# Kernel optimization log

Measured on AMD Instinct MI355X. Metric: run time of the kernel, lower is better.

## Reference

```python
import jax, jax.numpy as jnp
import numpy as np


def setup_inputs() -> dict:
    key = jax.random.key(0)
    k1, k2 = jax.random.split(key)
    inputs = jax.random.normal(k1, (32768, 512), dtype=jnp.float32)
    codebook = jax.random.normal(k2, (8192, 512), dtype=jnp.float32)
    return {"inputs": inputs, "codebook": codebook}


def reference(inputs, codebook):
    # inputs: [N, D] (flattened), codebook: [K, D]
    D = codebook.shape[1]
    x = inputs.reshape(-1, D)                          # [N, D]
    cb_sqr = jnp.sum(codebook ** 2, axis=1)            # [K]
    x_sqr = jnp.sum(x ** 2, axis=1, keepdims=True)     # [N, 1]
    distances = (cb_sqr[None, :] + x_sqr) - 2.0 * jnp.einsum('nd,kd->nk', x, codebook)
    soft_distances = jax.nn.softmax(-distances, axis=1)  # [N, K]
    return soft_distances
```

## Files before the change

kernel.cpp:

```cpp
#include <hip/hip_runtime.h>


typedef __attribute__((ext_vector_type(8))) __bf16 bf16x8;
typedef __attribute__((ext_vector_type(4))) float f32x4;

typedef __attribute__((address_space(1))) const void global_cvoid;
typedef __attribute__((address_space(3))) void lds_void;

__device__ inline unsigned short f32_to_bf16_rne(float f) {
    unsigned int u = __float_as_uint(f);
    unsigned int r = u + 0x7FFFu + ((u >> 16) & 1u);
    return (unsigned short)(r >> 16);
}
__device__ inline float bf16u_to_f32(unsigned short h) {
    return __uint_as_float(((unsigned int)h) << 16);
}

__global__ void split_kernel(const float* __restrict__ in,
                             unsigned short* __restrict__ hi,
                             unsigned short* __restrict__ lo, int n4) {
    int i = blockIdx.x * blockDim.x + threadIdx.x;
    int stride = gridDim.x * blockDim.x;
    for (; i < n4; i += stride) {
        float4 v = reinterpret_cast<const float4*>(in)[i];
        float vv[4] = {v.x, v.y, v.z, v.w};
        ushort4 hv, lv;
        unsigned short h[4], l[4];
#pragma unroll
        for (int j = 0; j < 4; ++j) {
            h[j] = f32_to_bf16_rne(vv[j]);
            float r = vv[j] - bf16u_to_f32(h[j]);
            l[j] = f32_to_bf16_rne(r);
        }
        hv.x = h[0]; hv.y = h[1]; hv.z = h[2]; hv.w = h[3];
        lv.x = l[0]; lv.y = l[1]; lv.z = l[2]; lv.w = l[3];
        reinterpret_cast<ushort4*>(hi)[i] = hv;
        reinterpret_cast<ushort4*>(lo)[i] = lv;
    }
}

__global__ void rowsq_kernel(const float* __restrict__ cb, float* __restrict__ out) {
    int row = blockIdx.x * 4 + (threadIdx.x >> 6);
    int lane = threadIdx.x & 63;
    const float4* p = reinterpret_cast<const float4*>(cb + (size_t)row * 512);
    float4 a = p[lane];
    float4 b = p[lane + 64];
    float s = a.x * a.x + a.y * a.y + a.z * a.z + a.w * a.w +
              b.x * b.x + b.y * b.y + b.z * b.z + b.w * b.w;
#pragma unroll
    for (int o = 32; o >= 1; o >>= 1) s += __shfl_xor(s, o);
    if (lane == 0) out[row] = s;
}


#define RD_A(mq_, kk_, b_)                                                        \
    { _Pragma("unroll") for (int m = 0; m < 4; ++m)                               \
        afr[m] = *(const bf16x8*)&lds[b_][0][kk_][(a_slot + ((mq_)*4 + m) * 64) * 8]; }

#define RD_B(kk_, b_)                                                             \
    { _Pragma("unroll") for (int n = 0; n < 4; ++n)                               \
        bfr[n] = *(const bf16x8*)&lds[b_][1][kk_][(b_slot + n * 64) * 8]; }

#define ST(mat_, kk_, b_, tt_)                                                    \
    { int prod_ = (tt_) >> 3, ch_ = (tt_) & 7;                                    \
      const unsigned short* bse_;                                                 \
      if ((mat_) == 0) bse_ = (prod_ < 2 ? Ah : Al) + arow0;                      \
      else             bse_ = (prod_ == 1 ? Bl : Bh) + brow0;                     \
      bse_ += ch_ * 64 + (kk_) * 32;                                              \
      _Pragma("unroll") for (int j = 0; j < 2; ++j)                               \
          __builtin_amdgcn_global_load_lds((global_cvoid*)(bse_ + goff[j]),       \
              (lds_void*)&lds[b_][mat_][kk_][sl8[j]], 16, 0, 0);                  \
    }

#define MM(mq_)                                                                   \
    { _Pragma("unroll") for (int m = 0; m < 4; ++m)                               \
      _Pragma("unroll") for (int n = 0; n < 4; ++n)                               \
          acc[(mq_) * 4 + m][n] = __builtin_amdgcn_mfma_f32_16x16x32_bf16(        \
              afr[m], bfr[n], acc[(mq_) * 4 + m][n], 0, 0, 0); }

#define MIDSYNC()                                                                 \
    { __builtin_amdgcn_s_barrier();                                               \
      asm volatile("s_waitcnt lgkmcnt(0)" ::: "memory"); }

template <int F16>
__global__ __launch_bounds__(512, 2) void gemm_kernel(
    const unsigned short* __restrict__ Ah, const unsigned short* __restrict__ Al,
    const unsigned short* __restrict__ Bh, const unsigned short* __restrict__ Bl,
    const float* __restrict__ cbq, float* __restrict__ outf,
    unsigned short* __restrict__ p16, float* __restrict__ max_part,
    float* __restrict__ sum_part) {
    __shared__ __align__(16) unsigned short lds[2][2][2][8192];

    const int t = threadIdx.x;
    const int lane = t & 63;
    const int w = t >> 6;
    const int wm = w >> 2, wn = w & 3;
    const int fr = lane & 15, fg = lane >> 4;

    int bid = blockIdx.x;
    int swz = (bid & 7) * 512 + (bid >> 3);
    const int bm = swz >> 5, bn = swz & 31;
    const int row0 = bm * 256, col0 = bn * 256;
    const size_t arow0 = (size_t)row0 * 512;
    const size_t brow0 = (size_t)col0 * 512;

    const int xsl = fg ^ ((fr >> 1) & 3);
    const int a_slot = (wm * 128 + fr) * 4 + xsl;
    const int b_slot = (wn * 64 + fr) * 4 + xsl;

    int goff[2], sl8[2];
#pragma unroll
    for (int j = 0; j < 2; ++j) {
        int s = j * 512 + t;
        int r_ = s >> 2, cp_ = s & 3;
        int cl_ = cp_ ^ ((r_ >> 1) & 3);
        goff[j] = r_ * 512 + cl_ * 8;
        sl8[j] = s * 8;
    }

    f32x4 acc[8][4] = {};
    bf16x8 afr[4], bfr[4];

    ST(0, 0, 0, 0);
    ST(1, 0, 0, 0);
    ST(0, 1, 0, 0);
    ST(1, 1, 0, 0);
    asm volatile("s_waitcnt vmcnt(4)\n\ts_barrier" ::: "memory");

    for (int tt = 0; tt < 24; ++tt) {
        const int cur = tt & 1, nb = cur ^ 1;
        const bool pf = (tt < 23);
        RD_B(0, cur);
        RD_A(0, 0, cur);
        if (pf) ST(0, 0, nb, tt + 1);
        MIDSYNC();
        __builtin_amdgcn_s_setprio(1); MM(0); __builtin_amdgcn_s_setprio(0);
        __builtin_amdgcn_s_barrier();
        RD_A(1, 0, cur);
        if (pf) ST(1, 0, nb, tt + 1);
        MIDSYNC();
        __builtin_amdgcn_s_setprio(1); MM(1); __builtin_amdgcn_s_setprio(0);
        if (pf) {
            asm volatile("s_waitcnt vmcnt(4)\n\ts_barrier" ::: "memory");
        } else {
            asm volatile("s_waitcnt vmcnt(0)\n\ts_barrier" ::: "memory");
        }
        RD_B(1, cur);
        RD_A(0, 1, cur);
        if (pf) ST(0, 1, nb, tt + 1);
        MIDSYNC();
        __builtin_amdgcn_s_setprio(1); MM(0); __builtin_amdgcn_s_setprio(0);
        __builtin_amdgcn_s_barrier();
        RD_A(1, 1, cur);
        if (pf) ST(1, 1, nb, tt + 1);
        MIDSYNC();
        __builtin_amdgcn_s_setprio(1); MM(1); __builtin_amdgcn_s_setprio(0);
        if (pf) {
            asm volatile("s_waitcnt vmcnt(4)\n\ts_barrier" ::: "memory");
        } else {
            __builtin_amdgcn_s_barrier();
        }
    }

    float* redm = (float*)&lds[0][0][0][0];
    float* reds = redm + 1024;

    float cq[4];
#pragma unroll
    for (int n = 0; n < 4; ++n) cq[n] = cbq[col0 + wn * 64 + n * 16 + fr];
#pragma unroll
    for (int m = 0; m < 8; ++m)
#pragma unroll
        for (int n = 0; n < 4; ++n)
#pragma unroll
            for (int r = 0; r < 4; ++r)
                acc[m][n][r] = 2.0f * acc[m][n][r] - cq[n];

    float rmx[8][4];
#pragma unroll
    for (int m = 0; m < 8; ++m)
#pragma unroll
        for (int r = 0; r < 4; ++r) {
            float v = fmaxf(fmaxf(acc[m][0][r], acc[m][1][r]),
                            fmaxf(acc[m][2][r], acc[m][3][r]));
#pragma unroll
            for (int o = 1; o < 16; o <<= 1) v = fmaxf(v, __shfl_xor(v, o));
            rmx[m][r] = v;
        }
    __syncthreads();
    if (fr == 0) {
#pragma unroll
        for (int m = 0; m < 8; ++m)
#pragma unroll
            for (int r = 0; r < 4; ++r)
                redm[wn * 256 + wm * 128 + m * 16 + fg * 4 + r] = rmx[m][r];
    }
    __syncthreads();
#pragma unroll
    for (int m = 0; m < 8; ++m)
#pragma unroll
        for (int r = 0; r < 4; ++r) {
            int row = wm * 128 + m * 16 + fg * 4 + r;
            rmx[m][r] = fmaxf(fmaxf(redm[row], redm[256 + row]),
                              fmaxf(redm[512 + row], redm[768 + row]));
        }
#pragma unroll
    for (int m = 0; m < 8; ++m)
#pragma unroll
        for (int r = 0; r < 4; ++r) {
            float s = 0.f;
#pragma unroll
            for (int n = 0; n < 4; ++n) s += __expf(acc[m][n][r] - rmx[m][r]);
#pragma unroll
            for (int o = 1; o < 16; o <<= 1) s += __shfl_xor(s, o);
            if (fr == 0) reds[wn * 256 + wm * 128 + m * 16 + fg * 4 + r] = s;
        }
    __syncthreads();
    if (wn == 0 && fr == 0) {
#pragma unroll
        for (int m = 0; m < 8; ++m)
#pragma unroll
            for (int r = 0; r < 4; ++r) {
                int row = wm * 128 + m * 16 + fg * 4 + r;
                size_t gr = (size_t)(row0 + row);
                max_part[gr * 32 + bn] = rmx[m][r];
                sum_part[gr * 32 + bn] =
                    reds[row] + reds[256 + row] + reds[512 + row] + reds[768 + row];
            }
    }
#pragma unroll
    for (int m = 0; m < 8; ++m)
#pragma unroll
        for (int n = 0; n < 4; ++n)
#pragma unroll
            for (int r = 0; r < 4; ++r) {
                size_t gr = (size_t)(row0 + wm * 128 + m * 16 + fg * 4 + r);
                size_t gi = gr * 8192 + col0 + wn * 64 + n * 16 + fr;
                if constexpr (F16) {
                    union { _Float16 h; unsigned short u; } cv;
                    cv.h = (_Float16)__expf(acc[m][n][r] - rmx[m][r]);
                    p16[gi] = cv.u;
                } else {
                    outf[gi] = acc[m][n][r];
                }
            }
}

__global__ void combine_kernel(const float* __restrict__ max_part,
                               const float* __restrict__ sum_part,
                               float* __restrict__ row_m, float* __restrict__ row_is,
                               float* __restrict__ scale, int do_scale) {
    int row = blockIdx.x * 8 + (threadIdx.x >> 5);
    int l = threadIdx.x & 31;
    size_t off = (size_t)row * 32 + l;
    float m = max_part[off];
    float s = sum_part[off];
    float gm = m;
#pragma unroll
    for (int o = 16; o >= 1; o >>= 1) gm = fmaxf(gm, __shfl_xor(gm, o, 32));
    float c = s * __expf(m - gm);
#pragma unroll
    for (int o = 16; o >= 1; o >>= 1) c += __shfl_xor(c, o, 32);
    float inv = 1.0f / c;
    if (do_scale) scale[off] = __expf(m - gm) * inv;
    if (l == 0) {
        row_m[row] = gm;
        row_is[row] = inv;
    }
}

__global__ void norm_kernel(float* __restrict__ out, const float* __restrict__ row_m,
                            const float* __restrict__ row_is) {
    size_t i = (size_t)blockIdx.x * blockDim.x + threadIdx.x;
    size_t stride = (size_t)gridDim.x * blockDim.x;
    const size_t n4 = 268435456ull / 4;
    float4* p = reinterpret_cast<float4*>(out);
    for (; i < n4; i += stride) {
        int row = (int)(i >> 11);
        float m = row_m[row];
        float is = row_is[row];
        float4 v = p[i];
        v.x = __expf(v.x - m) * is;
        v.y = __expf(v.y - m) * is;
        v.z = __expf(v.z - m) * is;
        v.w = __expf(v.w - m) * is;
        p[i] = v;
    }
}

__global__ void norm_f16_kernel(const unsigned short* __restrict__ p16,
                                const float* __restrict__ scale,
                                float* __restrict__ out) {
    size_t i = (size_t)blockIdx.x * blockDim.x + threadIdx.x;
    size_t stride = (size_t)gridDim.x * blockDim.x;
    const size_t ng = 268435456ull / 8;
    const uint4* src = reinterpret_cast<const uint4*>(p16);
    float4* dst = reinterpret_cast<float4*>(out);
    for (; i < ng; i += stride) {
        int row = (int)(i >> 10);
        int bn = (int)((i >> 5) & 31);
        float s = scale[(size_t)row * 32 + bn];
        union { uint4 u; _Float16 h[8]; } cv;
        cv.u = src[i];
        float4 o1, o2;
        o1.x = (float)cv.h[0] * s; o1.y = (float)cv.h[1] * s;
        o1.z = (float)cv.h[2] * s; o1.w = (float)cv.h[3] * s;
        o2.x = (float)cv.h[4] * s; o2.y = (float)cv.h[5] * s;
        o2.z = (float)cv.h[6] * s; o2.w = (float)cv.h[7] * s;
        dst[i * 2] = o1;
        dst[i * 2 + 1] = o2;
    }
}

extern "C" void kernel_launch(void* const* d_in, const int* in_sizes, int n_in,
                              void* d_out, int out_size, void* d_ws, size_t ws_size,
                              hipStream_t stream) {
    const float* x = (const float*)d_in[0];
    const float* cb = (const float*)d_in[1];
    float* out = (float*)d_out;
    char* ws = (char*)d_ws;

    unsigned short* Xh = (unsigned short*)(ws);
    unsigned short* Xl = (unsigned short*)(ws + 33554432ull);
    unsigned short* Ch = (unsigned short*)(ws + 67108864ull);
    unsigned short* Cl = (unsigned short*)(ws + 75497472ull);
    float* cbq       = (float*)(ws + 83886080ull);
    float* max_part  = (float*)(ws + 83918848ull);
    float* sum_part  = (float*)(ws + 88113152ull);
    float* row_m     = (float*)(ws + 92307456ull);
    float* row_is    = (float*)(ws + 92438528ull);
    float* scale     = (float*)(ws + 92569600ull);
    unsigned short* p16 = (unsigned short*)(ws + 96763904ull);

    const bool f16path = (ws_size >= 633634816ull);

    split_kernel<<<2048, 256, 0, stream>>>(x, Xh, Xl, 32768 * 512 / 4);
    split_kernel<<<1024, 256, 0, stream>>>(cb, Ch, Cl, 8192 * 512 / 4);
    rowsq_kernel<<<2048, 256, 0, stream>>>(cb, cbq);
    if (f16path) {
        gemm_kernel<1><<<4096, 512, 0, stream>>>(Xh, Xl, Ch, Cl, cbq, out, p16,
                                                 max_part, sum_part);
        combine_kernel<<<4096, 256, 0, stream>>>(max_part, sum_part, row_m, row_is,
                                                 scale, 1);
        norm_f16_kernel<<<4096, 256, 0, stream>>>(p16, scale, out);
    } else {
        gemm_kernel<0><<<4096, 512, 0, stream>>>(Xh, Xl, Ch, Cl, cbq, out, p16,
                                                 max_part, sum_part);
        combine_kernel<<<4096, 256, 0, stream>>>(max_part, sum_part, row_m, row_is,
                                                 scale, 0);
        norm_kernel<<<4096, 256, 0, stream>>>(out, row_m, row_is);
    }
}
```

Before: 1.380 ms.

## Deepen GEMM LDS pipeline to four stages with three tiles in flight

Replaces the double-buffered K-loop (two 32-wide sub-chunks per buffer) with a four-slot ring of 32-wide K chunks. Each step issues the A and B loads together three chunks ahead and waits with vmcnt(8), so more global-to-LDS loads are in flight while the MFMAs run. Total LDS size stays the same, but the loop now has 48 shorter iterations and a hand-tuned wait/barrier tail, which must stay correct for the last three chunks.

```diff
diff --git a/kernel.cpp b/kernel.cpp
--- a/kernel.cpp
+++ b/kernel.cpp
@@ -53,24 +53,24 @@
 }
 
 
-#define RD_A(mq_, kk_, b_)                                                        \
+#define RD_A(mq_, bq_)                                                            \
     { _Pragma("unroll") for (int m = 0; m < 4; ++m)                               \
-        afr[m] = *(const bf16x8*)&lds[b_][0][kk_][(a_slot + ((mq_)*4 + m) * 64) * 8]; }
-
-#define RD_B(kk_, b_)                                                             \
+        afr[m] = *(const bf16x8*)&lds[bq_][0][(a_slot + ((mq_)*4 + m) * 64) * 8]; }
+
+#define RD_B(bq_)                                                                 \
     { _Pragma("unroll") for (int n = 0; n < 4; ++n)                               \
-        bfr[n] = *(const bf16x8*)&lds[b_][1][kk_][(b_slot + n * 64) * 8]; }
-
-#define ST(mat_, kk_, b_, tt_)                                                    \
-    { int prod_ = (tt_) >> 3, ch_ = (tt_) & 7;                                    \
-      const unsigned short* bse_;                                                 \
-      if ((mat_) == 0) bse_ = (prod_ < 2 ? Ah : Al) + arow0;                      \
-      else             bse_ = (prod_ == 1 ? Bl : Bh) + brow0;                     \
-      bse_ += ch_ * 64 + (kk_) * 32;                                              \
-      _Pragma("unroll") for (int j = 0; j < 2; ++j)                               \
-          __builtin_amdgcn_global_load_lds((global_cvoid*)(bse_ + goff[j]),       \
-              (lds_void*)&lds[b_][mat_][kk_][sl8[j]], 16, 0, 0);                  \
-    }
+        bfr[n] = *(const bf16x8*)&lds[bq_][1][(b_slot + n * 64) * 8]; }
+
+#define ST(tt_)                                                                   \
+    { int prod_ = (tt_) >> 4, ko_ = ((tt_) & 15) * 32, bq_ = (tt_) & 3;           \
+      const unsigned short* Asrc_ = (prod_ < 2 ? Ah : Al) + arow0 + ko_;          \
+      const unsigned short* Bsrc_ = (prod_ == 1 ? Bl : Bh) + brow0 + ko_;         \
+      _Pragma("unroll") for (int j = 0; j < 2; ++j) {                             \
+          __builtin_amdgcn_global_load_lds((global_cvoid*)(Asrc_ + goff[j]),      \
+              (lds_void*)&lds[bq_][0][sl8[j]], 16, 0, 0);                         \
+          __builtin_amdgcn_global_load_lds((global_cvoid*)(Bsrc_ + goff[j]),      \
+              (lds_void*)&lds[bq_][1][sl8[j]], 16, 0, 0);                         \
+      } }
 
 #define MM(mq_)                                                                   \
     { _Pragma("unroll") for (int m = 0; m < 4; ++m)                               \
@@ -89,7 +89,7 @@
     const float* __restrict__ cbq, float* __restrict__ outf,
     unsigned short* __restrict__ p16, float* __restrict__ max_part,
     float* __restrict__ sum_part) {
-    __shared__ __align__(16) unsigned short lds[2][2][2][8192];
+    __shared__ __align__(16) unsigned short lds[4][2][8192];
 
     const int t = threadIdx.x;
     const int lane = t & 63;
@@ -121,48 +121,34 @@
     f32x4 acc[8][4] = {};
     bf16x8 afr[4], bfr[4];
 
-    ST(0, 0, 0, 0);
-    ST(1, 0, 0, 0);
-    ST(0, 1, 0, 0);
-    ST(1, 1, 0, 0);
-    asm volatile("s_waitcnt vmcnt(4)\n\ts_barrier" ::: "memory");
-
-    for (int tt = 0; tt < 24; ++tt) {
-        const int cur = tt & 1, nb = cur ^ 1;
-        const bool pf = (tt < 23);
-        RD_B(0, cur);
-        RD_A(0, 0, cur);
-        if (pf) ST(0, 0, nb, tt + 1);
+    ST(0);
+    ST(1);
+    ST(2);
+    asm volatile("s_waitcnt vmcnt(8)\n\ts_barrier" ::: "memory");
+
+    for (int tt = 0; tt < 48; ++tt) {
+        const int bq = tt & 3;
+        RD_B(bq);
+        RD_A(0, bq);
+        if (tt < 45) ST(tt + 3);
         MIDSYNC();
         __builtin_amdgcn_s_setprio(1); MM(0); __builtin_amdgcn_s_setprio(0);
         __builtin_amdgcn_s_barrier();
-        RD_A(1, 0, cur);
-        if (pf) ST(1, 0, nb, tt + 1);
+        RD_A(1, bq);
         MIDSYNC();
         __builtin_amdgcn_s_setprio(1); MM(1); __builtin_amdgcn_s_setprio(0);
-        if (pf) {
+        if (tt < 45) {
+            asm volatile("s_waitcnt vmcnt(8)\n\ts_barrier" ::: "memory");
+        } else if (tt == 45) {
             asm volatile("s_waitcnt vmcnt(4)\n\ts_barrier" ::: "memory");
-        } else {
+        } else if (tt == 46) {
             asm volatile("s_waitcnt vmcnt(0)\n\ts_barrier" ::: "memory");
-        }
-        RD_B(1, cur);
-        RD_A(0, 1, cur);
-        if (pf) ST(0, 1, nb, tt + 1);
-        MIDSYNC();
-        __builtin_amdgcn_s_setprio(1); MM(0); __builtin_amdgcn_s_setprio(0);
-        __builtin_amdgcn_s_barrier();
-        RD_A(1, 1, cur);
-        if (pf) ST(1, 1, nb, tt + 1);
-        MIDSYNC();
-        __builtin_amdgcn_s_setprio(1); MM(1); __builtin_amdgcn_s_setprio(0);
-        if (pf) {
-            asm volatile("s_waitcnt vmcnt(4)\n\ts_barrier" ::: "memory");
         } else {
             __builtin_amdgcn_s_barrier();
         }
     }
 
-    float* redm = (float*)&lds[0][0][0][0];
+    float* redm = (float*)&lds[0][0][0];
     float* reds = redm + 1024;
 
     float cq[4];
```

Measured after the change: 1.438 ms. +4.2%, slower.
